# Kernel optimization log

Hardware: AMD Instinct MI355X
Metric: run time of the kernel (lower is better)

## Reference

```python
import jax, jax.numpy as jnp
import numpy as np

WS = 7   # window size
SS = 3   # shift size
NH = 3   # num heads


def _rel_pos_index(ws):
    # [N, N] int index into (2*ws-1)^2 bias table, N = ws*ws
    coords = np.stack(np.meshgrid(np.arange(ws), np.arange(ws), indexing='ij')).reshape(2, -1)
    rel = coords[:, :, None] - coords[:, None, :]
    rel = rel.transpose(1, 2, 0).copy()
    rel[..., 0] += ws - 1
    rel[..., 1] += ws - 1
    rel[..., 0] *= 2 * ws - 1
    return rel.sum(-1)


def _attn_mask(H, W, ws, ss):
    # [nW, N, N] additive mask (0 / -1e9) for shifted windows
    img = np.zeros((H, W))
    cnt = 0
    slices = (slice(0, -ws), slice(-ws, -ss), slice(-ss, None))
    for h in slices:
        for w in slices:
            img[h, w] = cnt
            cnt += 1
    img = np.roll(img, (-ss, -ss), axis=(0, 1))
    mw = img.reshape(H // ws, ws, W // ws, ws).transpose(0, 2, 1, 3).reshape(-1, ws * ws)
    d = mw[:, None, :] - mw[:, :, None]
    return np.where(d != 0, -1e9, 0.0).astype(np.float32)


def setup_inputs() -> dict:
    key = jax.random.key(0)
    ks = jax.random.split(key, 6)
    B, H, W, C = 32, 112, 112, 96
    return {
        'x': jax.random.normal(ks[0], (B, H, W, C), jnp.float32),
        'qkv_w': jax.random.normal(ks[1], (C, 3 * C), jnp.float32) * 0.02,
        'qkv_b': jax.random.normal(ks[2], (3 * C,), jnp.float32) * 0.02,
        'proj_w': jax.random.normal(ks[3], (C, C), jnp.float32) * 0.02,
        'proj_b': jax.random.normal(ks[4], (C,), jnp.float32) * 0.02,
        'bias_table': jax.random.normal(ks[5], ((2 * WS - 1) ** 2, NH), jnp.float32) * 0.02,
    }


def reference(x, qkv_w, qkv_b, proj_w, proj_b, bias_table):
    B, H, W, C = x.shape
    ws, ss, nh = WS, SS, NH
    hd = C // nh
    scale = hd ** -0.5
    N = ws * ws
    # cyclic shift
    x = jnp.roll(x, (-ss, -ss), axis=(1, 2))
    # window partition -> [BnW, N, C]
    xw = x.reshape(B, H // ws, ws, W // ws, ws, C).transpose(0, 1, 3, 2, 4, 5).reshape(-1, N, C)
    BnW = xw.shape[0]
    qkv = (xw @ qkv_w + qkv_b).reshape(BnW, N, 3, nh, hd).transpose(2, 0, 3, 1, 4)
    q, k, v = qkv[0] * scale, qkv[1], qkv[2]  # [BnW, nh, N, hd]
    attn = jnp.einsum('bhnd,bhmd->bhnm', q, k)
    # relative position bias: gather [N*N] rows -> [nh, N, N]
    rel_idx = jnp.asarray(_rel_pos_index(ws))
    bias = bias_table[rel_idx.reshape(-1)].reshape(N, N, nh).transpose(2, 0, 1)
    attn = attn + bias[None]
    # shifted-window mask
    mask = jnp.asarray(_attn_mask(H, W, ws, ss))  # [nW, N, N]
    nW = mask.shape[0]
    attn = (attn.reshape(-1, nW, nh, N, N) + mask[None, :, None]).reshape(BnW, nh, N, N)
    attn = jax.nn.softmax(attn, axis=-1)
    out = jnp.einsum('bhnm,bhmd->bhnd', attn, v).transpose(0, 2, 1, 3).reshape(BnW, N, C)
    out = out @ proj_w + proj_b
    # window reverse + reverse shift
    xo = out.reshape(B, H // ws, W // ws, ws, ws, C).transpose(0, 1, 3, 2, 4, 5).reshape(B, H, W, C)
    return jnp.roll(xo, (ss, ss), axis=(1, 2))
```

## Files before the change

kernel.cpp:

```cpp
#include <hip/hip_runtime.h>

typedef __bf16 bf16x2 __attribute__((ext_vector_type(2)));
typedef __bf16 bf16x4 __attribute__((ext_vector_type(4)));
typedef __bf16 bf16x8 __attribute__((ext_vector_type(8)));
typedef float  f32x4  __attribute__((ext_vector_type(4)));

#define QKV_PACK_ELEMS 27648
#define PROJ_PACK_ELEMS 9216
#define TOTAL_PACK (QKV_PACK_ELEMS + PROJ_PACK_ELEMS)
#define BM_ELEMS (9 * 3 * 49 * 64)

#define LOG2E 1.4426950408889634f
#define QSCALE (0.17677669529663687f * 1.4426950408889634f)

__device__ __forceinline__ float fexp2(float x) {
    float r; asm("v_exp_f32 %0, %1" : "=v"(r) : "v"(x)); return r;
}

__device__ __forceinline__ int region1(int g) {
    return (g < 105) ? 0 : ((g < 109) ? 1 : 2);
}

__global__ __launch_bounds__(256) void prepack(
    const float* __restrict__ qkvw, const float* __restrict__ projw,
    const float* __restrict__ btab, __bf16* __restrict__ wp)
{
    int t = blockIdx.x * 256 + threadIdx.x;
    if (t < QKV_PACK_ELEMS) {
        int j = t & 7, lane = (t >> 3) & 63, g = t >> 9;
        int nt = g / 3, ks = g - 3 * nt;
        int k = ks * 32 + (lane >> 4) * 8 + j;
        int c = nt * 16 + (lane & 15);
        wp[t] = (__bf16)qkvw[k * 288 + c];
    } else if (t < TOTAL_PACK) {
        int t2 = t - QKV_PACK_ELEMS;
        int j = t2 & 7, lane = (t2 >> 3) & 63, g = t2 >> 9;
        int nt = g / 3, ks = g - 3 * nt;
        int k = ks * 32 + (lane >> 4) * 8 + j;
        int c = nt * 16 + (lane & 15);
        wp[t] = (__bf16)projw[k * 96 + c];
    } else if (t < TOTAL_PACK + BM_ELEMS) {
        int t2 = t - TOTAL_PACK;
        int k  = t2 & 63;
        int r  = t2 >> 6;
        int q  = r % 49;
        int r2 = r / 49;
        int h  = r2 % 3;
        int cls = r2 / 3;
        int rowcls = cls / 3, colcls = cls % 3;
        int wy = (rowcls == 0) ? 0 : (rowcls == 1 ? 14 : 15);
        int wx = (colcls == 0) ? 0 : (colcls == 1 ? 14 : 15);
        float val = -1e9f;
        if (k < 49) {
            int qi = q / 7, qj = q % 7, ki = k / 7, kj = k % 7;
            int rq = region1((wy * 7 + qi + 3) % 112) * 3 + region1((wx * 7 + qj + 3) % 112);
            int rk = region1((wy * 7 + ki + 3) % 112) * 3 + region1((wx * 7 + kj + 3) % 112);
            if (rq == rk)
                val = btab[((qi - ki + 6) * 13 + (qj - kj + 6)) * 3 + h] * LOG2E;
        }
        wp[TOTAL_PACK + t2] = (__bf16)val;
    }
}

__global__ __launch_bounds__(256, 4) void swmsa_fused(
    const float* __restrict__ xg,
    const __bf16* __restrict__ wp,
    const float* __restrict__ qkvb,
    const float* __restrict__ projb,
    float* __restrict__ outg)
{
    __shared__ __align__(16) char smem[31104];
    __bf16* xb  = (__bf16*)smem;
    __bf16* Qb  = (__bf16*)smem;
    __bf16* Pb  = (__bf16*)smem;
    __bf16* Kb  = (__bf16*)(smem + 9408);
    __bf16* Vt  = (__bf16*)(smem + 18816);

    const __bf16* wqkv  = wp;
    const __bf16* wproj = wp + QKV_PACK_ELEMS;
    const __bf16* bm    = wp + TOTAL_PACK;

    const int tid  = threadIdx.x;
    const int lane = tid & 63;
    const int wv   = tid >> 6;
    const int quad = lane >> 4;
    const int l16  = lane & 15;

    const int bw   = blockIdx.x;
    const int b    = bw >> 8;
    const int widx = bw & 255;
    const int wy   = widx >> 4, wx = widx & 15;
    const int h0   = wy * 7, w0 = wx * 7;

    for (int idx = tid; idx < 1176; idx += 256) {
        int n  = idx / 24;
        int c4 = idx - n * 24;
        int i = n / 7, j = n - 7 * i;
        int ho = h0 + i + 3; if (ho >= 112) ho -= 112;
        int wo = w0 + j + 3; if (wo >= 112) wo -= 112;
        const float4 v = *(const float4*)(xg + (size_t)((b * 112 + ho) * 112 + wo) * 96 + c4 * 4);
        bf16x4 p; p[0] = (__bf16)v.x; p[1] = (__bf16)v.y; p[2] = (__bf16)v.z; p[3] = (__bf16)v.w;
        *(bf16x4*)(xb + ((n * 96 + c4 * 4) ^ ((n & 3) << 3))) = p;
    }
    __syncthreads();

    {
        bf16x8 afr[4][3];
        #pragma unroll
        for (int mt = 0; mt < 4; mt++) {
            int row = mt * 16 + l16; if (row > 48) row = 48;
            #pragma unroll
            for (int ks = 0; ks < 3; ks++)
                afr[mt][ks] = *(const bf16x8*)(xb + ((row * 96 + ks * 32 + quad * 8) ^ ((row & 3) << 3)));
        }

        int nt = wv;
        bf16x8 b0 = *(const bf16x8*)(wqkv + ((nt * 3 + 0) << 9) + (lane << 3));
        bf16x8 b1 = *(const bf16x8*)(wqkv + ((nt * 3 + 1) << 9) + (lane << 3));
        bf16x8 b2 = *(const bf16x8*)(wqkv + ((nt * 3 + 2) << 9) + (lane << 3));
        float4 bias4 = *(const float4*)(qkvb + nt * 16 + quad * 4);
        float  biass = qkvb[nt * 16 + l16];
        __syncthreads();

        while (true) {
            const int ntn = nt + 4;
            const bool more = ntn < 18;
            bf16x8 nb0, nb1, nb2; float4 nbias4; float nbiass = 0.f;
            if (more) {
                nb0 = *(const bf16x8*)(wqkv + ((ntn * 3 + 0) << 9) + (lane << 3));
                nb1 = *(const bf16x8*)(wqkv + ((ntn * 3 + 1) << 9) + (lane << 3));
                nb2 = *(const bf16x8*)(wqkv + ((ntn * 3 + 2) << 9) + (lane << 3));
                nbias4 = *(const float4*)(qkvb + ntn * 16 + quad * 4);
                nbiass = qkvb[ntn * 16 + l16];
            }
            if (nt < 12) {
                #pragma unroll
                for (int mt = 0; mt < 4; mt++) {
                    f32x4 acc = {bias4.x, bias4.y, bias4.z, bias4.w};
                    acc = __builtin_amdgcn_mfma_f32_16x16x32_bf16(b0, afr[mt][0], acc, 0, 0, 0);
                    acc = __builtin_amdgcn_mfma_f32_16x16x32_bf16(b1, afr[mt][1], acc, 0, 0, 0);
                    acc = __builtin_amdgcn_mfma_f32_16x16x32_bf16(b2, afr[mt][2], acc, 0, 0, 0);
                    const int tok = mt * 16 + l16;
                    if (nt < 6) {
                        bf16x4 pk;
                        #pragma unroll
                        for (int r = 0; r < 4; r++) pk[r] = (__bf16)(acc[r] * QSCALE);
                        if (tok < 49)
                            *(bf16x4*)(Qb + ((tok * 96 + nt * 16 + quad * 4) ^ ((tok & 3) << 3))) = pk;
                    } else {
                        bf16x4 pk;
                        #pragma unroll
                        for (int r = 0; r < 4; r++) pk[r] = (__bf16)acc[r];
                        const int hh = (nt - 6) >> 1;
                        const int d0 = ((nt - 6) & 1) * 16;
                        if (tok < 49)
                            *(bf16x4*)(Kb + hh * 1568 + ((tok * 32 + d0 + quad * 4) ^ ((tok & 3) << 3))) = pk;
                    }
                }
            } else {
                const int c = nt * 16 + l16;
                const int cc = c - 192, hh = cc >> 5, d = cc & 31;
                #pragma unroll
                for (int mt = 0; mt < 4; mt++) {
                    f32x4 acc = {biass, biass, biass, biass};
                    acc = __builtin_amdgcn_mfma_f32_16x16x32_bf16(afr[mt][0], b0, acc, 0, 0, 0);
                    acc = __builtin_amdgcn_mfma_f32_16x16x32_bf16(afr[mt][1], b1, acc, 0, 0, 0);
                    acc = __builtin_amdgcn_mfma_f32_16x16x32_bf16(afr[mt][2], b2, acc, 0, 0, 0);
                    const int tokbase = mt * 16 + quad * 4;
                    bf16x4 pk;
                    #pragma unroll
                    for (int r = 0; r < 4; r++) {
                        int tok = tokbase + r;
                        pk[r] = (__bf16)((tok < 49) ? acc[r] : 0.f);
                    }
                    *(bf16x4*)(Vt + hh * 2048 + ((d * 64 + tokbase) ^ ((d & 7) << 3))) = pk;
                }
            }
            if (!more) break;
            b0 = nb0; b1 = nb1; b2 = nb2; bias4 = nbias4; biass = nbiass; nt = ntn;
        }
    }
    __syncthreads();

    int go[4];
    #pragma unroll
    for (int r = 0; r < 4; r++) {
        int t = 16 * wv + quad * 4 + r; if (t > 48) t = 48;
        int i = t / 7, j = t - 7 * i;
        int ho = h0 + i + 3; if (ho >= 112) ho -= 112;
        int wo = w0 + j + 3; if (wo >= 112) wo -= 112;
        go[r] = ((b * 112 + ho) * 112 + wo) * 96;
    }

    const int cls = ((wy < 14) ? 0 : (wy - 13)) * 3 + ((wx < 14) ? 0 : (wx - 13));
    const int qclamp = (16 * wv + l16 > 48) ? 48 : 16 * wv + l16;
    const __bf16* bmq = bm + ((size_t)(cls * 3) * 49 + qclamp) * 64;

    bf16x8 aq[3];
    #pragma unroll
    for (int h = 0; h < 3; h++)
        aq[h] = *(const bf16x8*)(Qb + ((qclamp * 96 + h * 32 + quad * 8) ^ ((qclamp & 3) << 3)));
    __syncthreads();

    __bf16* Pw = Pb + wv * 1152;
    __bf16* Ow = Pw;

    f32x4 pacc[6];
    #pragma unroll
    for (int nt = 0; nt < 6; nt++) {
        float pbias = projb[nt * 16 + l16];
        f32x4 t = {pbias, pbias, pbias, pbias};
        pacc[nt] = t;
    }

    #pragma unroll
    for (int h = 0; h < 3; h++) {
        const __bf16* Kh  = Kb + h * 1568;
        const __bf16* bmh = bmq + h * 49 * 64;
        f32x4 S[4];
        bf16x4 bmv[4];
        #pragma unroll
        for (int mt = 0; mt < 4; mt++) {
            int brow = mt * 16 + l16; if (brow > 48) brow = 48;
            bf16x8 bk = *(const bf16x8*)(Kh + ((brow * 32 + quad * 8) ^ ((brow & 3) << 3)));
            f32x4 z = {0.f, 0.f, 0.f, 0.f};
            S[mt] = __builtin_amdgcn_mfma_f32_16x16x32_bf16(bk, aq[h], z, 0, 0, 0);
            bmv[mt] = *(const bf16x4*)(bmh + mt * 16 + quad * 4);
        }
        float e[4][4];
        float sm0 = 0.f, sm1 = 0.f;
        #pragma unroll
        for (int mt = 0; mt < 4; mt++) {
            e[mt][0] = fexp2(S[mt][0] + (float)bmv[mt][0]);
            e[mt][1] = fexp2(S[mt][1] + (float)bmv[mt][1]);
            e[mt][2] = fexp2(S[mt][2] + (float)bmv[mt][2]);
            e[mt][3] = fexp2(S[mt][3] + (float)bmv[mt][3]);
            sm0 += e[mt][0] + e[mt][1];
            sm1 += e[mt][2] + e[mt][3];
        }
        float sm = sm0 + sm1;
        sm += __shfl_xor(sm, 16);
        sm += __shfl_xor(sm, 32);
        float rs = __builtin_amdgcn_rcpf(sm);
        #pragma unroll
        for (int mt = 0; mt < 4; mt++) {
            bf16x4 p;
            p[0] = (__bf16)(e[mt][0] * rs); p[1] = (__bf16)(e[mt][1] * rs);
            p[2] = (__bf16)(e[mt][2] * rs); p[3] = (__bf16)(e[mt][3] * rs);
            *(bf16x4*)(Pw + l16 * 72 + mt * 16 + quad * 4) = p;
        }
        bf16x8 pbf[6];
        #pragma unroll
        for (int nt = 0; nt < 6; nt++)
            pbf[nt] = *(const bf16x8*)(wproj + ((nt * 3 + h) << 9) + (lane << 3));
        {
            const __bf16* Vh = Vt + h * 2048;
            bf16x8 ap0 = *(const bf16x8*)(Pw + l16 * 72 + quad * 8);
            bf16x8 ap1 = *(const bf16x8*)(Pw + l16 * 72 + 32 + quad * 8);
            const int vsw = (l16 & 7) << 3;
            bf16x8 bv00 = *(const bf16x8*)(Vh + ((l16 * 64 + quad * 8) ^ vsw));
            bf16x8 bv01 = *(const bf16x8*)(Vh + ((l16 * 64 + 32 + quad * 8) ^ vsw));
            bf16x8 bv10 = *(const bf16x8*)(Vh + (((16 + l16) * 64 + quad * 8) ^ vsw));
            bf16x8 bv11 = *(const bf16x8*)(Vh + (((16 + l16) * 64 + 32 + quad * 8) ^ vsw));
            f32x4 O0 = {0.f, 0.f, 0.f, 0.f}, O1 = {0.f, 0.f, 0.f, 0.f};
            O0 = __builtin_amdgcn_mfma_f32_16x16x32_bf16(bv00, ap0, O0, 0, 0, 0);
            O0 = __builtin_amdgcn_mfma_f32_16x16x32_bf16(bv01, ap1, O0, 0, 0, 0);
            O1 = __builtin_amdgcn_mfma_f32_16x16x32_bf16(bv10, ap0, O1, 0, 0, 0);
            O1 = __builtin_amdgcn_mfma_f32_16x16x32_bf16(bv11, ap1, O1, 0, 0, 0);
            const int osw = (l16 & 3) << 3;
            bf16x4 o0, o1;
            #pragma unroll
            for (int r = 0; r < 4; r++) { o0[r] = (__bf16)O0[r]; o1[r] = (__bf16)O1[r]; }
            *(bf16x4*)(Ow + ((l16 * 32 + quad * 4) ^ osw))      = o0;
            *(bf16x4*)(Ow + ((l16 * 32 + 16 + quad * 4) ^ osw)) = o1;
            bf16x8 ao = *(const bf16x8*)(Ow + ((l16 * 32 + quad * 8) ^ osw));
            #pragma unroll
            for (int nt = 0; nt < 6; nt++)
                pacc[nt] = __builtin_amdgcn_mfma_f32_16x16x32_bf16(ao, pbf[nt], pacc[nt], 0, 0, 0);
        }
    }

    #pragma unroll
    for (int nt = 0; nt < 6; nt++) {
        const int c = nt * 16 + l16;
        #pragma unroll
        for (int r = 0; r < 4; r++) {
            int tok = 16 * wv + quad * 4 + r;
            if (tok < 49) outg[go[r] + c] = pacc[nt][r];
        }
    }
}

extern "C" void kernel_launch(void* const* d_in, const int* in_sizes, int n_in,
                              void* d_out, int out_size, void* d_ws, size_t ws_size,
                              hipStream_t stream) {
    const float* xg    = (const float*)d_in[0];
    const float* qkvw  = (const float*)d_in[1];
    const float* qkvb  = (const float*)d_in[2];
    const float* projw = (const float*)d_in[3];
    const float* projb = (const float*)d_in[4];
    const float* btab  = (const float*)d_in[5];
    float* outg = (float*)d_out;
    __bf16* wp = (__bf16*)d_ws;

    prepack<<<dim3((TOTAL_PACK + BM_ELEMS + 255) / 256), dim3(256), 0, stream>>>(
        qkvw, projw, btab, wp);
    swmsa_fused<<<dim3(8192), dim3(256), 0, stream>>>(xg, wp, qkvb, projb, outg);
}
```

Baseline: 338.3 us.

## Double-buffer per-head P tiles to interleave softmax with PV and projection

Splits the per-head loop into a score/softmax phase and a PV/projection phase, writing P into two alternating per-wave LDS buffers so head h+1's scores can be computed before head h's PV. This lets exp/softmax work overlap with MFMA chains across heads. It also changes the LDS swizzle to an XOR on bits (row>>1)&3 and drops the separate O swizzle by reusing the P buffer layout. LDS grows from about 31 KB to about 40 KB per block, which may reduce occupancy under the 4-blocks launch bound.

```diff
diff --git a/kernel.cpp b/kernel.cpp
--- a/kernel.cpp
+++ b/kernel.cpp
@@ -12,6 +12,8 @@
 
 #define LOG2E 1.4426950408889634f
 #define QSCALE (0.17677669529663687f * 1.4426950408889634f)
+
+#define SWZ2(row) ((((row) >> 1) & 3) << 3)
 
 __device__ __forceinline__ float fexp2(float x) {
     float r; asm("v_exp_f32 %0, %1" : "=v"(r) : "v"(x)); return r;
@@ -69,12 +71,11 @@
     const float* __restrict__ projb,
     float* __restrict__ outg)
 {
-    __shared__ __align__(16) char smem[31104];
+    __shared__ __align__(16) char smem[40320];
     __bf16* xb  = (__bf16*)smem;
     __bf16* Qb  = (__bf16*)smem;
-    __bf16* Pb  = (__bf16*)smem;
-    __bf16* Kb  = (__bf16*)(smem + 9408);
-    __bf16* Vt  = (__bf16*)(smem + 18816);
+    __bf16* Kb  = (__bf16*)(smem + 18624);
+    __bf16* Vt  = (__bf16*)(smem + 28032);
 
     const __bf16* wqkv  = wp;
     const __bf16* wproj = wp + QKV_PACK_ELEMS;
@@ -100,7 +101,7 @@
         int wo = w0 + j + 3; if (wo >= 112) wo -= 112;
         const float4 v = *(const float4*)(xg + (size_t)((b * 112 + ho) * 112 + wo) * 96 + c4 * 4);
         bf16x4 p; p[0] = (__bf16)v.x; p[1] = (__bf16)v.y; p[2] = (__bf16)v.z; p[3] = (__bf16)v.w;
-        *(bf16x4*)(xb + ((n * 96 + c4 * 4) ^ ((n & 3) << 3))) = p;
+        *(bf16x4*)(xb + ((n * 96 + c4 * 4) ^ SWZ2(n))) = p;
     }
     __syncthreads();
 
@@ -111,7 +112,7 @@
             int row = mt * 16 + l16; if (row > 48) row = 48;
             #pragma unroll
             for (int ks = 0; ks < 3; ks++)
-                afr[mt][ks] = *(const bf16x8*)(xb + ((row * 96 + ks * 32 + quad * 8) ^ ((row & 3) << 3)));
+                afr[mt][ks] = *(const bf16x8*)(xb + ((row * 96 + ks * 32 + quad * 8) ^ SWZ2(row)));
         }
 
         int nt = wv;
@@ -146,7 +147,7 @@
                         #pragma unroll
                         for (int r = 0; r < 4; r++) pk[r] = (__bf16)(acc[r] * QSCALE);
                         if (tok < 49)
-                            *(bf16x4*)(Qb + ((tok * 96 + nt * 16 + quad * 4) ^ ((tok & 3) << 3))) = pk;
+                            *(bf16x4*)(Qb + ((tok * 96 + nt * 16 + quad * 4) ^ SWZ2(tok))) = pk;
                     } else {
                         bf16x4 pk;
                         #pragma unroll
@@ -154,7 +155,7 @@
                         const int hh = (nt - 6) >> 1;
                         const int d0 = ((nt - 6) & 1) * 16;
                         if (tok < 49)
-                            *(bf16x4*)(Kb + hh * 1568 + ((tok * 32 + d0 + quad * 4) ^ ((tok & 3) << 3))) = pk;
+                            *(bf16x4*)(Kb + hh * 1568 + ((tok * 32 + d0 + quad * 4) ^ SWZ2(tok))) = pk;
                     }
                 }
             } else {
@@ -199,11 +200,11 @@
     bf16x8 aq[3];
     #pragma unroll
     for (int h = 0; h < 3; h++)
-        aq[h] = *(const bf16x8*)(Qb + ((qclamp * 96 + h * 32 + quad * 8) ^ ((qclamp & 3) << 3)));
+        aq[h] = *(const bf16x8*)(Qb + ((qclamp * 96 + h * 32 + quad * 8) ^ SWZ2(qclamp)));
     __syncthreads();
 
-    __bf16* Pw = Pb + wv * 1152;
-    __bf16* Ow = Pw;
+    __bf16* Pb0 = (__bf16*)smem + wv * 1152;
+    __bf16* Pb1 = (__bf16*)(smem + 9408) + wv * 1152;
 
     f32x4 pacc[6];
     #pragma unroll
@@ -213,8 +214,7 @@
         pacc[nt] = t;
     }
 
-    #pragma unroll
-    for (int h = 0; h < 3; h++) {
+    auto compS = [&](int h, __bf16* Pdst) {
         const __bf16* Kh  = Kb + h * 1568;
         const __bf16* bmh = bmq + h * 49 * 64;
         f32x4 S[4];
@@ -222,7 +222,7 @@
         #pragma unroll
         for (int mt = 0; mt < 4; mt++) {
             int brow = mt * 16 + l16; if (brow > 48) brow = 48;
-            bf16x8 bk = *(const bf16x8*)(Kh + ((brow * 32 + quad * 8) ^ ((brow & 3) << 3)));
+            bf16x8 bk = *(const bf16x8*)(Kh + ((brow * 32 + quad * 8) ^ SWZ2(brow)));
             f32x4 z = {0.f, 0.f, 0.f, 0.f};
             S[mt] = __builtin_amdgcn_mfma_f32_16x16x32_bf16(bk, aq[h], z, 0, 0, 0);
             bmv[mt] = *(const bf16x4*)(bmh + mt * 16 + quad * 4);
@@ -247,38 +247,45 @@
             bf16x4 p;
             p[0] = (__bf16)(e[mt][0] * rs); p[1] = (__bf16)(e[mt][1] * rs);
             p[2] = (__bf16)(e[mt][2] * rs); p[3] = (__bf16)(e[mt][3] * rs);
-            *(bf16x4*)(Pw + l16 * 72 + mt * 16 + quad * 4) = p;
-        }
+            *(bf16x4*)(Pdst + l16 * 72 + mt * 16 + quad * 4) = p;
+        }
+    };
+
+    auto finishH = [&](int h, __bf16* Pbuf) {
+        bf16x8 ap0 = *(const bf16x8*)(Pbuf + l16 * 72 + quad * 8);
+        bf16x8 ap1 = *(const bf16x8*)(Pbuf + l16 * 72 + 32 + quad * 8);
         bf16x8 pbf[6];
         #pragma unroll
         for (int nt = 0; nt < 6; nt++)
             pbf[nt] = *(const bf16x8*)(wproj + ((nt * 3 + h) << 9) + (lane << 3));
-        {
-            const __bf16* Vh = Vt + h * 2048;
-            bf16x8 ap0 = *(const bf16x8*)(Pw + l16 * 72 + quad * 8);
-            bf16x8 ap1 = *(const bf16x8*)(Pw + l16 * 72 + 32 + quad * 8);
-            const int vsw = (l16 & 7) << 3;
-            bf16x8 bv00 = *(const bf16x8*)(Vh + ((l16 * 64 + quad * 8) ^ vsw));
-            bf16x8 bv01 = *(const bf16x8*)(Vh + ((l16 * 64 + 32 + quad * 8) ^ vsw));
-            bf16x8 bv10 = *(const bf16x8*)(Vh + (((16 + l16) * 64 + quad * 8) ^ vsw));
-            bf16x8 bv11 = *(const bf16x8*)(Vh + (((16 + l16) * 64 + 32 + quad * 8) ^ vsw));
-            f32x4 O0 = {0.f, 0.f, 0.f, 0.f}, O1 = {0.f, 0.f, 0.f, 0.f};
-            O0 = __builtin_amdgcn_mfma_f32_16x16x32_bf16(bv00, ap0, O0, 0, 0, 0);
-            O0 = __builtin_amdgcn_mfma_f32_16x16x32_bf16(bv01, ap1, O0, 0, 0, 0);
-            O1 = __builtin_amdgcn_mfma_f32_16x16x32_bf16(bv10, ap0, O1, 0, 0, 0);
-            O1 = __builtin_amdgcn_mfma_f32_16x16x32_bf16(bv11, ap1, O1, 0, 0, 0);
-            const int osw = (l16 & 3) << 3;
-            bf16x4 o0, o1;
-            #pragma unroll
-            for (int r = 0; r < 4; r++) { o0[r] = (__bf16)O0[r]; o1[r] = (__bf16)O1[r]; }
-            *(bf16x4*)(Ow + ((l16 * 32 + quad * 4) ^ osw))      = o0;
-            *(bf16x4*)(Ow + ((l16 * 32 + 16 + quad * 4) ^ osw)) = o1;
-            bf16x8 ao = *(const bf16x8*)(Ow + ((l16 * 32 + quad * 8) ^ osw));
-            #pragma unroll
-            for (int nt = 0; nt < 6; nt++)
-                pacc[nt] = __builtin_amdgcn_mfma_f32_16x16x32_bf16(ao, pbf[nt], pacc[nt], 0, 0, 0);
-        }
-    }
+        const __bf16* Vh = Vt + h * 2048;
+        const int vsw = (l16 & 7) << 3;
+        bf16x8 bv00 = *(const bf16x8*)(Vh + ((l16 * 64 + quad * 8) ^ vsw));
+        bf16x8 bv01 = *(const bf16x8*)(Vh + ((l16 * 64 + 32 + quad * 8) ^ vsw));
+        bf16x8 bv10 = *(const bf16x8*)(Vh + (((16 + l16) * 64 + quad * 8) ^ vsw));
+        bf16x8 bv11 = *(const bf16x8*)(Vh + (((16 + l16) * 64 + 32 + quad * 8) ^ vsw));
+        f32x4 O0 = {0.f, 0.f, 0.f, 0.f}, O1 = {0.f, 0.f, 0.f, 0.f};
+        O0 = __builtin_amdgcn_mfma_f32_16x16x32_bf16(bv00, ap0, O0, 0, 0, 0);
+        O0 = __builtin_amdgcn_mfma_f32_16x16x32_bf16(bv01, ap1, O0, 0, 0, 0);
+        O1 = __builtin_amdgcn_mfma_f32_16x16x32_bf16(bv10, ap0, O1, 0, 0, 0);
+        O1 = __builtin_amdgcn_mfma_f32_16x16x32_bf16(bv11, ap1, O1, 0, 0, 0);
+        bf16x4 o0, o1;
+        #pragma unroll
+        for (int r = 0; r < 4; r++) { o0[r] = (__bf16)O0[r]; o1[r] = (__bf16)O1[r]; }
+        *(bf16x4*)(Pbuf + l16 * 72 + quad * 4)      = o0;
+        *(bf16x4*)(Pbuf + l16 * 72 + 16 + quad * 4) = o1;
+        bf16x8 ao = *(const bf16x8*)(Pbuf + l16 * 72 + quad * 8);
+        #pragma unroll
+        for (int nt = 0; nt < 6; nt++)
+            pacc[nt] = __builtin_amdgcn_mfma_f32_16x16x32_bf16(ao, pbf[nt], pacc[nt], 0, 0, 0);
+    };
+
+    compS(0, Pb0);
+    compS(1, Pb1);
+    finishH(0, Pb0);
+    compS(2, Pb0);
+    finishH(1, Pb1);
+    finishH(2, Pb0);
 
     #pragma unroll
     for (int nt = 0; nt < 6; nt++) {
```

Result: no change. 343.5 us (+1.5%).

## Separate Q/K/V shared buffers to drop barriers, defer softmax normalization

Applied to the files above, without the earlier changes.

Gives the x tile, Q, K and V their own shared-memory regions instead of aliasing them. This removes two __syncthreads barriers that guarded buffer reuse, at the cost of a larger LDS footprint (about 40 KB per block), which may lower occupancy relative to the launch bound of 4 blocks. The softmax reciprocal is now applied to the PV output instead of to every probability, so fewer multiplies happen before the shared-memory store. The change also uses a different swizzle pattern and sets s_setprio around the MFMA sections.

```diff
diff --git a/kernel.cpp b/kernel.cpp
--- a/kernel.cpp
+++ b/kernel.cpp
@@ -12,6 +12,8 @@
 
 #define LOG2E 1.4426950408889634f
 #define QSCALE (0.17677669529663687f * 1.4426950408889634f)
+
+#define SWZ2(row) ((((row) >> 1) & 3) << 3)
 
 __device__ __forceinline__ float fexp2(float x) {
     float r; asm("v_exp_f32 %0, %1" : "=v"(r) : "v"(x)); return r;
@@ -69,12 +71,11 @@
     const float* __restrict__ projb,
     float* __restrict__ outg)
 {
-    __shared__ __align__(16) char smem[31104];
+    __shared__ __align__(16) char smem[40512];
     __bf16* xb  = (__bf16*)smem;
-    __bf16* Qb  = (__bf16*)smem;
-    __bf16* Pb  = (__bf16*)smem;
-    __bf16* Kb  = (__bf16*)(smem + 9408);
-    __bf16* Vt  = (__bf16*)(smem + 18816);
+    __bf16* Qb  = (__bf16*)(smem + 9408);
+    __bf16* Kb  = (__bf16*)(smem + 18816);
+    __bf16* Vt  = (__bf16*)(smem + 28224);
 
     const __bf16* wqkv  = wp;
     const __bf16* wproj = wp + QKV_PACK_ELEMS;
@@ -100,7 +101,7 @@
         int wo = w0 + j + 3; if (wo >= 112) wo -= 112;
         const float4 v = *(const float4*)(xg + (size_t)((b * 112 + ho) * 112 + wo) * 96 + c4 * 4);
         bf16x4 p; p[0] = (__bf16)v.x; p[1] = (__bf16)v.y; p[2] = (__bf16)v.z; p[3] = (__bf16)v.w;
-        *(bf16x4*)(xb + ((n * 96 + c4 * 4) ^ ((n & 3) << 3))) = p;
+        *(bf16x4*)(xb + ((n * 96 + c4 * 4) ^ SWZ2(n))) = p;
     }
     __syncthreads();
 
@@ -111,7 +112,7 @@
             int row = mt * 16 + l16; if (row > 48) row = 48;
             #pragma unroll
             for (int ks = 0; ks < 3; ks++)
-                afr[mt][ks] = *(const bf16x8*)(xb + ((row * 96 + ks * 32 + quad * 8) ^ ((row & 3) << 3)));
+                afr[mt][ks] = *(const bf16x8*)(xb + ((row * 96 + ks * 32 + quad * 8) ^ SWZ2(row)));
         }
 
         int nt = wv;
@@ -120,7 +121,6 @@
         bf16x8 b2 = *(const bf16x8*)(wqkv + ((nt * 3 + 2) << 9) + (lane << 3));
         float4 bias4 = *(const float4*)(qkvb + nt * 16 + quad * 4);
         float  biass = qkvb[nt * 16 + l16];
-        __syncthreads();
 
         while (true) {
             const int ntn = nt + 4;
@@ -146,7 +146,7 @@
                         #pragma unroll
                         for (int r = 0; r < 4; r++) pk[r] = (__bf16)(acc[r] * QSCALE);
                         if (tok < 49)
-                            *(bf16x4*)(Qb + ((tok * 96 + nt * 16 + quad * 4) ^ ((tok & 3) << 3))) = pk;
+                            *(bf16x4*)(Qb + ((tok * 96 + nt * 16 + quad * 4) ^ SWZ2(tok))) = pk;
                     } else {
                         bf16x4 pk;
                         #pragma unroll
@@ -154,7 +154,7 @@
                         const int hh = (nt - 6) >> 1;
                         const int d0 = ((nt - 6) & 1) * 16;
                         if (tok < 49)
-                            *(bf16x4*)(Kb + hh * 1568 + ((tok * 32 + d0 + quad * 4) ^ ((tok & 3) << 3))) = pk;
+                            *(bf16x4*)(Kb + hh * 1568 + ((tok * 32 + d0 + quad * 4) ^ SWZ2(tok))) = pk;
                     }
                 }
             } else {
@@ -199,11 +199,9 @@
     bf16x8 aq[3];
     #pragma unroll
     for (int h = 0; h < 3; h++)
-        aq[h] = *(const bf16x8*)(Qb + ((qclamp * 96 + h * 32 + quad * 8) ^ ((qclamp & 3) << 3)));
-    __syncthreads();
-
-    __bf16* Pw = Pb + wv * 1152;
-    __bf16* Ow = Pw;
+        aq[h] = *(const bf16x8*)(Qb + ((qclamp * 96 + h * 32 + quad * 8) ^ SWZ2(qclamp)));
+
+    __bf16* Pw = (__bf16*)smem + wv * 1152;
 
     f32x4 pacc[6];
     #pragma unroll
@@ -219,14 +217,16 @@
         const __bf16* bmh = bmq + h * 49 * 64;
         f32x4 S[4];
         bf16x4 bmv[4];
+        __builtin_amdgcn_s_setprio(1);
         #pragma unroll
         for (int mt = 0; mt < 4; mt++) {
             int brow = mt * 16 + l16; if (brow > 48) brow = 48;
-            bf16x8 bk = *(const bf16x8*)(Kh + ((brow * 32 + quad * 8) ^ ((brow & 3) << 3)));
+            bf16x8 bk = *(const bf16x8*)(Kh + ((brow * 32 + quad * 8) ^ SWZ2(brow)));
             f32x4 z = {0.f, 0.f, 0.f, 0.f};
             S[mt] = __builtin_amdgcn_mfma_f32_16x16x32_bf16(bk, aq[h], z, 0, 0, 0);
             bmv[mt] = *(const bf16x4*)(bmh + mt * 16 + quad * 4);
         }
+        __builtin_amdgcn_s_setprio(0);
         float e[4][4];
         float sm0 = 0.f, sm1 = 0.f;
         #pragma unroll
@@ -238,17 +238,17 @@
             sm0 += e[mt][0] + e[mt][1];
             sm1 += e[mt][2] + e[mt][3];
         }
+        #pragma unroll
+        for (int mt = 0; mt < 4; mt++) {
+            bf16x4 p;
+            p[0] = (__bf16)e[mt][0]; p[1] = (__bf16)e[mt][1];
+            p[2] = (__bf16)e[mt][2]; p[3] = (__bf16)e[mt][3];
+            *(bf16x4*)(Pw + l16 * 72 + mt * 16 + quad * 4) = p;
+        }
         float sm = sm0 + sm1;
         sm += __shfl_xor(sm, 16);
         sm += __shfl_xor(sm, 32);
         float rs = __builtin_amdgcn_rcpf(sm);
-        #pragma unroll
-        for (int mt = 0; mt < 4; mt++) {
-            bf16x4 p;
-            p[0] = (__bf16)(e[mt][0] * rs); p[1] = (__bf16)(e[mt][1] * rs);
-            p[2] = (__bf16)(e[mt][2] * rs); p[3] = (__bf16)(e[mt][3] * rs);
-            *(bf16x4*)(Pw + l16 * 72 + mt * 16 + quad * 4) = p;
-        }
         bf16x8 pbf[6];
         #pragma unroll
         for (int nt = 0; nt < 6; nt++)
@@ -263,20 +263,26 @@
             bf16x8 bv10 = *(const bf16x8*)(Vh + (((16 + l16) * 64 + quad * 8) ^ vsw));
             bf16x8 bv11 = *(const bf16x8*)(Vh + (((16 + l16) * 64 + 32 + quad * 8) ^ vsw));
             f32x4 O0 = {0.f, 0.f, 0.f, 0.f}, O1 = {0.f, 0.f, 0.f, 0.f};
+            __builtin_amdgcn_s_setprio(1);
             O0 = __builtin_amdgcn_mfma_f32_16x16x32_bf16(bv00, ap0, O0, 0, 0, 0);
             O0 = __builtin_amdgcn_mfma_f32_16x16x32_bf16(bv01, ap1, O0, 0, 0, 0);
             O1 = __builtin_amdgcn_mfma_f32_16x16x32_bf16(bv10, ap0, O1, 0, 0, 0);
             O1 = __builtin_amdgcn_mfma_f32_16x16x32_bf16(bv11, ap1, O1, 0, 0, 0);
-            const int osw = (l16 & 3) << 3;
+            __builtin_amdgcn_s_setprio(0);
             bf16x4 o0, o1;
             #pragma unroll
-            for (int r = 0; r < 4; r++) { o0[r] = (__bf16)O0[r]; o1[r] = (__bf16)O1[r]; }
-            *(bf16x4*)(Ow + ((l16 * 32 + quad * 4) ^ osw))      = o0;
-            *(bf16x4*)(Ow + ((l16 * 32 + 16 + quad * 4) ^ osw)) = o1;
-            bf16x8 ao = *(const bf16x8*)(Ow + ((l16 * 32 + quad * 8) ^ osw));
+            for (int r = 0; r < 4; r++) {
+                o0[r] = (__bf16)(O0[r] * rs);
+                o1[r] = (__bf16)(O1[r] * rs);
+            }
+            *(bf16x4*)(Pw + l16 * 72 + quad * 4)      = o0;
+            *(bf16x4*)(Pw + l16 * 72 + 16 + quad * 4) = o1;
+            bf16x8 ao = *(const bf16x8*)(Pw + l16 * 72 + quad * 8);
+            __builtin_amdgcn_s_setprio(1);
             #pragma unroll
             for (int nt = 0; nt < 6; nt++)
                 pacc[nt] = __builtin_amdgcn_mfma_f32_16x16x32_bf16(ao, pbf[nt], pacc[nt], 0, 0, 0);
+            __builtin_amdgcn_s_setprio(0);
         }
     }
 
```

After: 340.7 us. No clear change (+0.7%).
